# Performance work log

Measured on AMD Instinct MI355X. Metric: run time of the kernel, lower is better.

## Reference

```python
import jax, jax.numpy as jnp
import numpy as np

B, QL, KL = 2, 1024, 4096
H = 1024          # hidden_size
NH = 16           # num_heads
HD = H // NH      # head_dim = 64


def setup_inputs() -> dict:
    key = jax.random.key(0)
    k1, k2, k3, k4, k5 = jax.random.split(key, 5)
    s = 1.0 / np.sqrt(H)
    return {
        "query": jax.random.normal(k1, (B, QL, H), dtype=jnp.float32),
        "key_value": jax.random.normal(k2, (B, KL, H), dtype=jnp.float32),
        "w_q": jax.random.uniform(k3, (H, H), dtype=jnp.float32, minval=-s, maxval=s),
        "w_kv": jax.random.uniform(k4, (H, 2 * H), dtype=jnp.float32, minval=-s, maxval=s),
        "w_out": jax.random.uniform(k5, (H, H), dtype=jnp.float32, minval=-s, maxval=s),
    }


def reference(query, key_value, w_q, w_kv, w_out):
    # projections
    q = (query @ w_q).reshape(B, QL, NH, HD).transpose(0, 2, 1, 3)      # [B,NH,QL,HD]
    kv = (key_value @ w_kv).reshape(B, KL, 2, NH, HD)
    k = kv[:, :, 0].transpose(0, 2, 1, 3)                               # [B,NH,KL,HD]
    v = kv[:, :, 1].transpose(0, 2, 1, 3)                               # [B,NH,KL,HD]
    # scaled dot-product attention (explicit, matching source)
    scale = 1.0 / np.sqrt(HD).astype(np.float32)
    attn = jnp.einsum("bhqd,bhkd->bhqk", q, k) * scale                  # [B,NH,QL,KL]
    attn = jax.nn.softmax(attn, axis=-1)
    out = jnp.einsum("bhqk,bhkd->bhqd", attn, v)                        # [B,NH,QL,HD]
    out = out.transpose(0, 2, 1, 3).reshape(B, QL, H)
    return out @ w_out
```

## Files before the change

### kernel.cpp

```cpp
#include <hip/hip_runtime.h>

#define Bb   2
#define QL   1024
#define KL   4096
#define Hh   1024
#define NH   16
#define HD   64

#define KSPLIT 2
#define CHUNK  (KL / KSPLIT)
#define NTT    (CHUNK / 64)

typedef unsigned short u16;
typedef __attribute__((ext_vector_type(8))) short bf16x8;
typedef __attribute__((ext_vector_type(8))) unsigned short usv8;
typedef __attribute__((ext_vector_type(4))) float f32x4;

#define QSCALE 0.1803368801111204f
#define RTHR   11.0f

__device__ __forceinline__ u16 f2bf(float f) {
    union { float f; unsigned int u; } v; v.f = f;
    unsigned int r = (v.u + 0x7FFFu + ((v.u >> 16) & 1u)) >> 16;
    return (u16)r;
}

__device__ __forceinline__ unsigned int cvt_pk_bf16(float lo, float hi) {
    unsigned int r;
    asm("v_cvt_pk_bf16_f32 %0, %1, %2" : "=v"(r) : "v"(lo), "v"(hi));
    return r;
}

__device__ __forceinline__ float max3f(float a, float b, float c) {
    float r;
    asm("v_max3_f32 %0, %1, %2, %3" : "=v"(r) : "v"(a), "v"(b), "v"(c));
    return r;
}

__device__ __forceinline__ void gload16(const void* g, void* l) {
    __builtin_amdgcn_global_load_lds(
        (const __attribute__((address_space(1))) void*)g,
        (__attribute__((address_space(3))) void*)l, 16, 0, 0);
}

__device__ __forceinline__ uint4 pack8(const float4& f0, const float4& f1) {
    uint4 o;
    o.x = cvt_pk_bf16(f0.x, f0.y);
    o.y = cvt_pk_bf16(f0.z, f0.w);
    o.z = cvt_pk_bf16(f1.x, f1.y);
    o.w = cvt_pk_bf16(f1.z, f1.w);
    return o;
}

__global__ __launch_bounds__(256) void wtrans_all(const float* __restrict__ wq,
                                                  const float* __restrict__ wkv,
                                                  const float* __restrict__ wout,
                                                  u16* __restrict__ wqT,
                                                  u16* __restrict__ wkvT,
                                                  u16* __restrict__ woutT) {
    __shared__ float T[64][65];
    int bid = blockIdx.x;
    const float* in; u16* out; int C;
    if (bid < 256)      { in = wq;   out = wqT;   C = 1024; }
    else if (bid < 768) { in = wkv;  out = wkvT;  C = 2048; bid -= 256; }
    else                { in = wout; out = woutT; C = 1024; bid -= 768; }
    const int nc = C >> 6;
    const int c0 = (bid % nc) * 64;
    const int r0 = (bid / nc) * 64;
    const int t  = threadIdx.x;
    const int tx = t & 15, ty = t >> 4;
#pragma unroll
    for (int p = 0; p < 4; ++p) {
        const int r = ty + p * 16;
        float4 v = *reinterpret_cast<const float4*>(in + (size_t)(r0 + r) * C + c0 + tx * 4);
        T[r][tx * 4 + 0] = v.x; T[r][tx * 4 + 1] = v.y;
        T[r][tx * 4 + 2] = v.z; T[r][tx * 4 + 3] = v.w;
    }
    __syncthreads();
#pragma unroll
    for (int p = 0; p < 4; ++p) {
        const int c = ty + p * 16;
        const int n = c0 + c;
        ushort4 o;
        o.x = f2bf(T[tx * 4 + 0][c]); o.y = f2bf(T[tx * 4 + 1][c]);
        o.z = f2bf(T[tx * 4 + 2][c]); o.w = f2bf(T[tx * 4 + 3][c]);
        const int kb   = r0 + tx * 4;
        const int kout = (kb & ~63) | ((((kb >> 3) & 7) ^ (n & 7)) << 3) | (kb & 7);
        *reinterpret_cast<ushort4*>(out + (size_t)n * 1024 + kout) = o;
    }
}

__global__ __launch_bounds__(256) void qgemm(const float* __restrict__ A32,
                                             const u16* __restrict__ Bt,
                                             u16* __restrict__ C) {
    __shared__ u16 As[64 * 64];
    __shared__ u16 Bs[128 * 64];
    const int nwg = gridDim.x * gridDim.y;
    const int id  = blockIdx.y * gridDim.x + blockIdx.x;
    const int sw  = (id & 7) * (nwg >> 3) + (id >> 3);
    const int bx  = sw % gridDim.x, by = sw / gridDim.x;
    const int tid = threadIdx.x, lane = tid & 63, w = tid >> 6;
    const int wr = w >> 1, wc = w & 1;
    const int row0 = by * 64, col0 = bx * 128;
    const int MROW = wr * 32;
    const int x7   = lane & 7;

    f32x4 acc[2][4];
#pragma unroll
    for (int m = 0; m < 2; ++m)
#pragma unroll
        for (int n = 0; n < 4; ++n) acc[m][n] = (f32x4){0.f, 0.f, 0.f, 0.f};

    const int lrow = lane >> 3, lcol = (lane & 7) * 8;
    const int arow = tid >> 3, acol8 = (tid & 7) * 8;
    const int aphys = acol8 ^ ((arow & 7) << 3);

    for (int k0 = 0; k0 < 1024; k0 += 64) {
        __syncthreads();
#pragma unroll
        for (int p = 0; p < 2; ++p) {
            const int r = p * 32 + arow;
            const float* src = A32 + (size_t)(row0 + r) * 1024 + k0 + acol8;
            float4 f0 = *reinterpret_cast<const float4*>(src);
            float4 f1 = *reinterpret_cast<const float4*>(src + 4);
            *reinterpret_cast<uint4*>(&As[r * 64 + aphys]) = pack8(f0, f1);
        }
#pragma unroll
        for (int p = 0; p < 4; ++p) {
            const int base = w * 512 + p * 2048;
            const int row  = (base >> 6) + lrow;
            gload16(Bt + (size_t)(col0 + row) * 1024 + k0 + lcol, &Bs[base]);
        }
        __syncthreads();
#pragma unroll
        for (int kk = 0; kk < 2; ++kk) {
            bf16x8 af[2], bfr[4];
            const int G = ((kk * 4 + (lane >> 4)) ^ x7) * 8;
#pragma unroll
            for (int m = 0; m < 2; ++m)
                af[m] = *reinterpret_cast<const bf16x8*>(
                    &As[(MROW + m * 16 + (lane & 15)) * 64 + G]);
#pragma unroll
            for (int n = 0; n < 4; ++n)
                bfr[n] = *reinterpret_cast<const bf16x8*>(
                    &Bs[(wc * 64 + n * 16 + (lane & 15)) * 64 + G]);
#pragma unroll
            for (int m = 0; m < 2; ++m)
#pragma unroll
                for (int n = 0; n < 4; ++n)
                    acc[m][n] = __builtin_amdgcn_mfma_f32_16x16x32_bf16(
                        af[m], bfr[n], acc[m][n], 0, 0, 0);
        }
    }
#pragma unroll
    for (int m = 0; m < 2; ++m)
#pragma unroll
        for (int n = 0; n < 4; ++n) {
            const int gc = col0 + wc * 64 + n * 16 + (lane & 15);
#pragma unroll
            for (int r = 0; r < 4; ++r) {
                const int gr = row0 + MROW + m * 16 + (lane >> 4) * 4 + r;
                C[(size_t)gr * 1024 + gc] = f2bf(acc[m][n][r] * QSCALE);
            }
        }
}

__global__ __launch_bounds__(256) void kvgemm(const float* __restrict__ A32,
                                              const u16* __restrict__ Bt,
                                              u16* __restrict__ KT,
                                              u16* __restrict__ VT) {
    __shared__ u16 As[128 * 64];
    __shared__ u16 Bs[128 * 64];
    const int nwg = gridDim.x * gridDim.y;
    const int id  = blockIdx.y * gridDim.x + blockIdx.x;
    const int sw  = (id & 7) * (nwg >> 3) + (id >> 3);
    const int bx  = sw % gridDim.x, by = sw / gridDim.x;
    const int tid = threadIdx.x, lane = tid & 63, w = tid >> 6;
    const int wr = w >> 1, wc = w & 1;
    const int row0 = by * 128, col0 = bx * 128;
    const int MROW = wr * 64;
    const int x7   = lane & 7;

    f32x4 acc[4][4];
#pragma unroll
    for (int m = 0; m < 4; ++m)
#pragma unroll
        for (int n = 0; n < 4; ++n) acc[m][n] = (f32x4){0.f, 0.f, 0.f, 0.f};

    const int lrow = lane >> 3, lcol = (lane & 7) * 8;
    const int arow = tid >> 3, acol8 = (tid & 7) * 8;
    const int aphys = acol8 ^ ((arow & 7) << 3);

    auto stage = [&](int k0) {
        __syncthreads();
#pragma unroll
        for (int p = 0; p < 4; ++p) {
            const int r = p * 32 + arow;
            const float* src = A32 + (size_t)(row0 + r) * 1024 + k0 + acol8;
            float4 f0 = *reinterpret_cast<const float4*>(src);
            float4 f1 = *reinterpret_cast<const float4*>(src + 4);
            *reinterpret_cast<uint4*>(&As[r * 64 + aphys]) = pack8(f0, f1);
        }
#pragma unroll
        for (int p = 0; p < 4; ++p) {
            const int base = w * 512 + p * 2048;
            const int row  = (base >> 6) + lrow;
            gload16(Bt + (size_t)(col0 + row) * 1024 + k0 + lcol, &Bs[base]);
        }
        __syncthreads();
    };

    if (col0 < 1024) {
        for (int k0 = 0; k0 < 1024; k0 += 64) {
            stage(k0);
#pragma unroll
            for (int kk = 0; kk < 2; ++kk) {
                bf16x8 af[4], bfr[4];
                const int G = ((kk * 4 + (lane >> 4)) ^ x7) * 8;
#pragma unroll
                for (int m = 0; m < 4; ++m)
                    af[m] = *reinterpret_cast<const bf16x8*>(
                        &As[(MROW + m * 16 + (lane & 15)) * 64 + G]);
#pragma unroll
                for (int n = 0; n < 4; ++n)
                    bfr[n] = *reinterpret_cast<const bf16x8*>(
                        &Bs[(wc * 64 + n * 16 + (lane & 15)) * 64 + G]);
#pragma unroll
                for (int m = 0; m < 4; ++m)
#pragma unroll
                    for (int n = 0; n < 4; ++n)
                        acc[m][n] = __builtin_amdgcn_mfma_f32_16x16x32_bf16(
                            bfr[n], af[m], acc[m][n], 0, 0, 0);
            }
        }
#pragma unroll
        for (int m = 0; m < 4; ++m) {
            const int gr  = row0 + MROW + m * 16 + (lane & 15);
            const int b   = gr >> 12;
            const int k   = gr & 4095;
            const int kt_i = k >> 6, k_in = k & 63;
#pragma unroll
            for (int n = 0; n < 4; ++n) {
                const int gc0 = col0 + wc * 64 + n * 16 + (lane >> 4) * 4;
                const int h   = gc0 >> 6, d0 = gc0 & 63;
                u16* blob = KT + (((size_t)((b << 4) + h) * 64 + kt_i) << 9) * 8;
                const int og = k_in * 8 + ((d0 >> 3) ^ (k_in & 7));
                ushort4 pk;
                pk.x = f2bf(acc[m][n][0]); pk.y = f2bf(acc[m][n][1]);
                pk.z = f2bf(acc[m][n][2]); pk.w = f2bf(acc[m][n][3]);
                *reinterpret_cast<ushort4*>(&blob[og * 8 + (d0 & 7)]) = pk;
            }
        }
    } else {
        for (int k0 = 0; k0 < 1024; k0 += 64) {
            stage(k0);
#pragma unroll
            for (int kk = 0; kk < 2; ++kk) {
                bf16x8 af[4], bfr[4];
                const int G = ((kk * 4 + (lane >> 4)) ^ x7) * 8;
#pragma unroll
                for (int m = 0; m < 4; ++m)
                    af[m] = *reinterpret_cast<const bf16x8*>(
                        &As[(MROW + m * 16 + (lane & 15)) * 64 + G]);
#pragma unroll
                for (int n = 0; n < 4; ++n)
                    bfr[n] = *reinterpret_cast<const bf16x8*>(
                        &Bs[(wc * 64 + n * 16 + (lane & 15)) * 64 + G]);
#pragma unroll
                for (int m = 0; m < 4; ++m)
#pragma unroll
                    for (int n = 0; n < 4; ++n)
                        acc[m][n] = __builtin_amdgcn_mfma_f32_16x16x32_bf16(
                            af[m], bfr[n], acc[m][n], 0, 0, 0);
            }
        }
#pragma unroll
        for (int m = 0; m < 4; ++m) {
            const int gr0 = row0 + MROW + m * 16 + (lane >> 4) * 4;
            const int b   = gr0 >> 12;
            const int k   = gr0 & 4095;
            const int kt_i = k >> 6, k_in = k & 63;
#pragma unroll
            for (int n = 0; n < 4; ++n) {
                const int gc = col0 + wc * 64 + n * 16 + (lane & 15);
                const int h  = (gc & 1023) >> 6, d = gc & 63;
                u16* blob = VT + (((size_t)((b << 4) + h) * 64 + kt_i) << 9) * 8;
                const int og = d * 8 + ((k_in >> 3) ^ (d & 7));
                ushort4 pk;
                pk.x = f2bf(acc[m][n][0]); pk.y = f2bf(acc[m][n][1]);
                pk.z = f2bf(acc[m][n][2]); pk.w = f2bf(acc[m][n][3]);
                *reinterpret_cast<ushort4*>(&blob[og * 8 + (k_in & 7)]) = pk;
            }
        }
    }
}

__global__ __launch_bounds__(256, 4) void attn_mfma(const u16* __restrict__ Qb,
                                                    const u16* __restrict__ KT,
                                                    const u16* __restrict__ VT2,
                                                    float* __restrict__ Op,
                                                    float* __restrict__ m_ws,
                                                    float* __restrict__ l_ws) {
    __shared__ u16 Ks[2][64 * 64];
    __shared__ u16 Vs[2][64 * 64];
    __shared__ u16 Ps[4][16][64];

    const int bid0 = blockIdx.x;
    const int bid  = (bid0 & 7) * 128 + (bid0 >> 3);
    const int qb   = bid & 15;
    const int h    = (bid >> 4) & 15;
    const int b    = (bid >> 8) & 1;
    const int c    = bid >> 9;
    const int tid  = threadIdx.x;
    const int lane = tid & 63;
    const int w    = tid >> 6;
    const int q_l  = lane & 15;
    const int g    = lane >> 4;
    const int qs7  = q_l & 7;
    const int q0   = qb * 64;
    const int bh   = b * NH + h;

    bf16x8 qa0, qa1;
    {
        const u16* qsrc = Qb + (size_t)(b * QL + q0 + w * 16 + q_l) * Hh
                          + h * HD + g * 8;
        qa0 = *reinterpret_cast<const bf16x8*>(qsrc);
        qa1 = *reinterpret_cast<const bf16x8*>(qsrc + 32);
    }
    asm volatile("s_waitcnt vmcnt(0)" ::: "memory");

    bf16x8 ones;
#pragma unroll
    for (int e = 0; e < 8; ++e) ones[e] = (short)0x3F80;

    float m_i = -1e30f;
    f32x4 acc_l = (f32x4){0.f, 0.f, 0.f, 0.f};
    f32x4 acc_o[4];
#pragma unroll
    for (int n = 0; n < 4; ++n) acc_o[n] = (f32x4){0.f, 0.f, 0.f, 0.f};

    const size_t tb0 = ((size_t)bh * 64 + c * NTT) * 512 * 8;
    const u16* kq = KT  + tb0;
    const u16* vq = VT2 + tb0;

    auto issue = [&](const u16* kptr, const u16* vptr, int bufi) {
#pragma unroll
        for (int p = 0; p < 2; ++p)
            gload16(kptr + (size_t)(p * 256 + w * 64 + lane) * 8,
                    &Ks[bufi][(p * 256 + w * 64) * 8]);
#pragma unroll
        for (int p = 0; p < 2; ++p)
            gload16(vptr + (size_t)(p * 256 + w * 64 + lane) * 8,
                    &Vs[bufi][(p * 256 + w * 64) * 8]);
    };

    issue(kq, vq, 0);

    for (int t = 0; t < NTT; ++t) {
        const int cur = t & 1;
        __builtin_amdgcn_s_barrier();
        if (t + 1 < NTT) {
            kq += 4096; vq += 4096;
            issue(kq, vq, cur ^ 1);
            asm volatile("s_waitcnt vmcnt(4)" ::: "memory");
        } else {
            asm volatile("s_waitcnt vmcnt(0)" ::: "memory");
        }
        __builtin_amdgcn_sched_barrier(0);
        __builtin_amdgcn_s_barrier();

        f32x4 s[4];
        __builtin_amdgcn_s_setprio(1);
#pragma unroll
        for (int n = 0; n < 4; ++n) {
            const int r_ = n * 16 + q_l;
            bf16x8 a0 = *reinterpret_cast<const bf16x8*>(
                &Ks[cur][r_ * 64 + (g ^ qs7) * 8]);
            bf16x8 a1 = *reinterpret_cast<const bf16x8*>(
                &Ks[cur][r_ * 64 + ((g + 4) ^ qs7) * 8]);
            f32x4 z = (f32x4){0.f, 0.f, 0.f, 0.f};
            z = __builtin_amdgcn_mfma_f32_16x16x32_bf16(a0, qa0, z, 0, 0, 0);
            z = __builtin_amdgcn_mfma_f32_16x16x32_bf16(a1, qa1, z, 0, 0, 0);
            s[n] = z;
        }
        __builtin_amdgcn_s_setprio(0);

        float c1 = max3f(s[0][0], s[0][1], s[0][2]);
        c1 = max3f(c1, s[0][3], s[1][0]);
        c1 = max3f(c1, s[1][1], s[1][2]);
        c1 = fmaxf(c1, s[1][3]);
        float c2 = max3f(s[2][0], s[2][1], s[2][2]);
        c2 = max3f(c2, s[2][3], s[3][0]);
        c2 = max3f(c2, s[3][1], s[3][2]);
        c2 = fmaxf(c2, s[3][3]);
        float mloc = fmaxf(c1, c2);
        mloc = fmaxf(mloc, __shfl_xor(mloc, 16));
        mloc = fmaxf(mloc, __shfl_xor(mloc, 32));

        if (__any(mloc > m_i + RTHR)) {
            const float mnew = fmaxf(m_i, mloc);
            const float al   = exp2f(m_i - mnew);
            m_i = mnew;
            acc_l[0] *= al; acc_l[1] *= al; acc_l[2] *= al; acc_l[3] *= al;
#pragma unroll
            for (int n = 0; n < 4; ++n) {
                f32x4 tt = acc_o[n];
                tt[0] *= al; tt[1] *= al; tt[2] *= al; tt[3] *= al;
                acc_o[n] = tt;
            }
        }
#pragma unroll
        for (int n = 0; n < 4; ++n)
#pragma unroll
            for (int r = 0; r < 4; ++r) s[n][r] = exp2f(s[n][r] - m_i);

#pragma unroll
        for (int n = 0; n < 4; ++n) {
            uint2 pk2;
            pk2.x = cvt_pk_bf16(s[n][0], s[n][1]);
            pk2.y = cvt_pk_bf16(s[n][2], s[n][3]);
            const int phys = (2 * n + (g >> 1)) ^ qs7;
            *reinterpret_cast<uint2*>(&Ps[w][q_l][phys * 8 + (g & 1) * 4]) = pk2;
        }
        asm volatile("s_waitcnt lgkmcnt(0)" ::: "memory");
        __builtin_amdgcn_sched_barrier(0);

        __builtin_amdgcn_s_setprio(1);
#pragma unroll
        for (int kf = 0; kf < 2; ++kf) {
            const int phk = ((kf * 4 + g) ^ qs7) * 8;
            bf16x8 pfr = *reinterpret_cast<const bf16x8*>(&Ps[w][q_l][phk]);
            acc_l = __builtin_amdgcn_mfma_f32_16x16x32_bf16(ones, pfr, acc_l, 0, 0, 0);
#pragma unroll
            for (int n = 0; n < 4; ++n) {
                const int d_ = n * 16 + q_l;
                bf16x8 vf = *reinterpret_cast<const bf16x8*>(
                    &Vs[cur][d_ * 64 + phk]);
                acc_o[n] = __builtin_amdgcn_mfma_f32_16x16x32_bf16(
                    vf, pfr, acc_o[n], 0, 0, 0);
            }
        }
        __builtin_amdgcn_s_setprio(0);
    }

    float* opc = Op + (size_t)c * ((size_t)Bb * QL * Hh)
                 + (size_t)(b * QL + q0 + w * 16 + q_l) * Hh + h * HD;
#pragma unroll
    for (int n = 0; n < 4; ++n) {
        float4 v = make_float4(acc_o[n][0], acc_o[n][1], acc_o[n][2], acc_o[n][3]);
        *reinterpret_cast<float4*>(opc + n * 16 + g * 4) = v;
    }
    if (g == 0) {
        const int idx = ((c * Bb + b) * NH + h) * QL + q0 + w * 16 + q_l;
        m_ws[idx] = m_i;
        l_ws[idx] = acc_l[0];
    }
}

__global__ __launch_bounds__(256) void ogemm(const float* __restrict__ Op,
                                             const float* __restrict__ m_ws,
                                             const float* __restrict__ l_ws,
                                             const u16* __restrict__ Bt,
                                             float* __restrict__ C) {
    __shared__ u16 As[64 * 64];
    __shared__ u16 Bs[128 * 64];
    const int nwg = gridDim.x * gridDim.y;
    const int id  = blockIdx.y * gridDim.x + blockIdx.x;
    const int sw  = (id & 7) * (nwg >> 3) + (id >> 3);
    const int bx  = sw % gridDim.x, by = sw / gridDim.x;
    const int tid = threadIdx.x, lane = tid & 63, w = tid >> 6;
    const int wr = w >> 1, wc = w & 1;
    const int row0 = by * 64, col0 = bx * 128;
    const int MROW = wr * 32;
    const int x7   = lane & 7;

    f32x4 acc[2][4];
#pragma unroll
    for (int m = 0; m < 2; ++m)
#pragma unroll
        for (int n = 0; n < 4; ++n) acc[m][n] = (f32x4){0.f, 0.f, 0.f, 0.f};

    const int lrow = lane >> 3, lcol = (lane & 7) * 8;
    const int arow = tid >> 3, acol8 = (tid & 7) * 8;
    const int aphys = acol8 ^ ((arow & 7) << 3);

    for (int k0 = 0; k0 < 1024; k0 += 64) {
        __syncthreads();
        const int h_ = k0 >> 6;
#pragma unroll
        for (int p = 0; p < 2; ++p) {
            const int r    = p * 32 + arow;
            const int grow = row0 + r;
            const int b_   = grow >> 10, q_ = grow & 1023;
            const int idx  = (((b_ << 4) + h_) << 10) + q_;
            const float m0 = m_ws[idx], m1 = m_ws[idx + 32768];
            const float l0 = l_ws[idx], l1 = l_ws[idx + 32768];
            const float ms = fmaxf(m0, m1);
            float a0 = exp2f(m0 - ms), a1 = exp2f(m1 - ms);
            const float inv = 1.f / (l0 * a0 + l1 * a1);
            a0 *= inv; a1 *= inv;
            const float* o0 = Op + (size_t)grow * 1024 + k0 + acol8;
            const float* o1 = o0 + (size_t)Bb * QL * Hh;
            float4 x0 = *reinterpret_cast<const float4*>(o0);
            float4 x1 = *reinterpret_cast<const float4*>(o0 + 4);
            float4 y0 = *reinterpret_cast<const float4*>(o1);
            float4 y1 = *reinterpret_cast<const float4*>(o1 + 4);
            float4 f0 = make_float4(x0.x * a0 + y0.x * a1, x0.y * a0 + y0.y * a1,
                                    x0.z * a0 + y0.z * a1, x0.w * a0 + y0.w * a1);
            float4 f1 = make_float4(x1.x * a0 + y1.x * a1, x1.y * a0 + y1.y * a1,
                                    x1.z * a0 + y1.z * a1, x1.w * a0 + y1.w * a1);
            *reinterpret_cast<uint4*>(&As[r * 64 + aphys]) = pack8(f0, f1);
        }
#pragma unroll
        for (int p = 0; p < 4; ++p) {
            const int base = w * 512 + p * 2048;
            const int row  = (base >> 6) + lrow;
            gload16(Bt + (size_t)(col0 + row) * 1024 + k0 + lcol, &Bs[base]);
        }
        __syncthreads();
#pragma unroll
        for (int kk = 0; kk < 2; ++kk) {
            bf16x8 af[2], bfr[4];
            const int G = ((kk * 4 + (lane >> 4)) ^ x7) * 8;
#pragma unroll
            for (int m = 0; m < 2; ++m)
                af[m] = *reinterpret_cast<const bf16x8*>(
                    &As[(MROW + m * 16 + (lane & 15)) * 64 + G]);
#pragma unroll
            for (int n = 0; n < 4; ++n)
                bfr[n] = *reinterpret_cast<const bf16x8*>(
                    &Bs[(wc * 64 + n * 16 + (lane & 15)) * 64 + G]);
#pragma unroll
            for (int m = 0; m < 2; ++m)
#pragma unroll
                for (int n = 0; n < 4; ++n)
                    acc[m][n] = __builtin_amdgcn_mfma_f32_16x16x32_bf16(
                        af[m], bfr[n], acc[m][n], 0, 0, 0);
        }
    }
#pragma unroll
    for (int m = 0; m < 2; ++m)
#pragma unroll
        for (int n = 0; n < 4; ++n) {
            const int gc = col0 + wc * 64 + n * 16 + (lane & 15);
#pragma unroll
            for (int r = 0; r < 4; ++r) {
                const int gr = row0 + MROW + m * 16 + (lane >> 4) * 4 + r;
                C[(size_t)gr * 1024 + gc] = acc[m][n][r];
            }
        }
}

extern "C" void kernel_launch(void* const* d_in, const int* in_sizes, int n_in,
                              void* d_out, int out_size, void* d_ws, size_t ws_size,
                              hipStream_t stream) {
    const float* query     = (const float*)d_in[0];
    const float* key_value = (const float*)d_in[1];
    const float* w_q       = (const float*)d_in[2];
    const float* w_kv      = (const float*)d_in[3];
    const float* w_out     = (const float*)d_in[4];
    float* out = (float*)d_out;

    char* ws = (char*)d_ws;
    const size_t MB = 1024 * 1024;
    u16*   KT    = (u16*)(ws);
    u16*   VT    = (u16*)(ws + 16 * MB);
    float* Opart = (float*)(ws + 32 * MB);
    u16*   Qb    = (u16*)(ws + 48 * MB);
    u16*   wkvT  = (u16*)(ws + 52 * MB);
    u16*   wqT   = (u16*)(ws + 56 * MB);
    u16*   woutT = (u16*)(ws + 58 * MB);
    float* m_wsp = (float*)(ws + 60 * MB);
    float* l_wsp = (float*)(ws + 60 * MB + 256 * 1024);

    dim3 blk(256);

    wtrans_all<<<1024, blk, 0, stream>>>(w_q, w_kv, w_out, wqT, wkvT, woutT);

    qgemm<<<dim3(8, 32), blk, 0, stream>>>(query, wqT, Qb);

    kvgemm<<<dim3(16, 64), blk, 0, stream>>>(key_value, wkvT, KT, VT);

    attn_mfma<<<dim3(KSPLIT * 512), blk, 0, stream>>>(
        Qb, KT, VT, Opart, m_wsp, l_wsp);

    ogemm<<<dim3(8, 32), blk, 0, stream>>>(Opart, m_wsp, l_wsp, woutT, out);
}
```

Baseline: 183.7 us.

## Process two query sub-tiles per wave in attention to reuse K/V fragments

Each attention block now covers 128 query rows instead of 64, with each wave handling two 16-row query sub-tiles that share the same K and V LDS fragment loads. This halves the grid and the global K/V traffic per query, and lowers LDS reads per MFMA. LDS addresses are precomputed as pointers and the loop is unrolled by two to fix the buffer index. The cost is roughly double the accumulator registers (launch bounds go from 4 to 2 waves per SIMD) and fewer blocks, which lowers occupancy and leaves less latency hiding.

```diff
diff --git a/kernel.cpp b/kernel.cpp
--- a/kernel.cpp
+++ b/kernel.cpp
@@ -295,37 +295,38 @@
     }
 }
 
-__global__ __launch_bounds__(256, 4) void attn_mfma(const u16* __restrict__ Qb,
+__global__ __launch_bounds__(256, 2) void attn_mfma(const u16* __restrict__ Qb,
                                                     const u16* __restrict__ KT,
                                                     const u16* __restrict__ VT2,
                                                     float* __restrict__ Op,
                                                     float* __restrict__ m_ws,
                                                     float* __restrict__ l_ws) {
-    __shared__ u16 Ks[2][64 * 64];
-    __shared__ u16 Vs[2][64 * 64];
-    __shared__ u16 Ps[4][16][64];
+    __shared__ u16 Ks[2][4096];
+    __shared__ u16 Vs[2][4096];
+    __shared__ u16 Ps[4][2][1024];
 
     const int bid0 = blockIdx.x;
-    const int bid  = (bid0 & 7) * 128 + (bid0 >> 3);
-    const int qb   = bid & 15;
-    const int h    = (bid >> 4) & 15;
-    const int b    = (bid >> 8) & 1;
-    const int c    = bid >> 9;
+    const int bid  = (bid0 & 7) * 64 + (bid0 >> 3);
+    const int qb   = bid & 7;
+    const int h    = (bid >> 3) & 15;
+    const int b    = (bid >> 7) & 1;
+    const int c    = bid >> 8;
     const int tid  = threadIdx.x;
     const int lane = tid & 63;
     const int w    = tid >> 6;
     const int q_l  = lane & 15;
     const int g    = lane >> 4;
     const int qs7  = q_l & 7;
-    const int q0   = qb * 64;
+    const int q0   = qb * 128;
     const int bh   = b * NH + h;
 
-    bf16x8 qa0, qa1;
-    {
-        const u16* qsrc = Qb + (size_t)(b * QL + q0 + w * 16 + q_l) * Hh
+    bf16x8 qa[2][2];
+#pragma unroll
+    for (int qh = 0; qh < 2; ++qh) {
+        const u16* qsrc = Qb + (size_t)(b * QL + q0 + w * 32 + qh * 16 + q_l) * Hh
                           + h * HD + g * 8;
-        qa0 = *reinterpret_cast<const bf16x8*>(qsrc);
-        qa1 = *reinterpret_cast<const bf16x8*>(qsrc + 32);
+        qa[qh][0] = *reinterpret_cast<const bf16x8*>(qsrc);
+        qa[qh][1] = *reinterpret_cast<const bf16x8*>(qsrc + 32);
     }
     asm volatile("s_waitcnt vmcnt(0)" ::: "memory");
 
@@ -333,35 +334,47 @@
 #pragma unroll
     for (int e = 0; e < 8; ++e) ones[e] = (short)0x3F80;
 
-    float m_i = -1e30f;
-    f32x4 acc_l = (f32x4){0.f, 0.f, 0.f, 0.f};
-    f32x4 acc_o[4];
-#pragma unroll
-    for (int n = 0; n < 4; ++n) acc_o[n] = (f32x4){0.f, 0.f, 0.f, 0.f};
-
-    const size_t tb0 = ((size_t)bh * 64 + c * NTT) * 512 * 8;
-    const u16* kq = KT  + tb0;
-    const u16* vq = VT2 + tb0;
-
-    auto issue = [&](const u16* kptr, const u16* vptr, int bufi) {
-#pragma unroll
-        for (int p = 0; p < 2; ++p)
-            gload16(kptr + (size_t)(p * 256 + w * 64 + lane) * 8,
-                    &Ks[bufi][(p * 256 + w * 64) * 8]);
-#pragma unroll
-        for (int p = 0; p < 2; ++p)
-            gload16(vptr + (size_t)(p * 256 + w * 64 + lane) * 8,
-                    &Vs[bufi][(p * 256 + w * 64) * 8]);
-    };
-
-    issue(kq, vq, 0);
-
-    for (int t = 0; t < NTT; ++t) {
-        const int cur = t & 1;
+    float m_i[2] = {-1e30f, -1e30f};
+    f32x4 acc_l[2] = {(f32x4){0.f, 0.f, 0.f, 0.f}, (f32x4){0.f, 0.f, 0.f, 0.f}};
+    f32x4 acc_o[2][4];
+#pragma unroll
+    for (int qh = 0; qh < 2; ++qh)
+#pragma unroll
+        for (int n = 0; n < 4; ++n) acc_o[qh][n] = (f32x4){0.f, 0.f, 0.f, 0.f};
+
+    const int koffA = (g ^ qs7) * 8;
+    const int koffB = ((g + 4) ^ qs7) * 8;
+    const int rowq  = q_l * 64;
+    const u16* KsA[2] = { &Ks[0][rowq + koffA], &Ks[1][rowq + koffA] };
+    const u16* KsB[2] = { &Ks[0][rowq + koffB], &Ks[1][rowq + koffB] };
+    const u16* VsA[2] = { &Vs[0][rowq + koffA], &Vs[1][rowq + koffA] };
+    const u16* VsB[2] = { &Vs[0][rowq + koffB], &Vs[1][rowq + koffB] };
+    const u16* PsRA = &Ps[w][0][rowq + koffA];
+    const u16* PsRB = &Ps[w][0][rowq + koffB];
+    u16* PsW[4];
+#pragma unroll
+    for (int n = 0; n < 4; ++n)
+        PsW[n] = &Ps[w][0][rowq + (((2 * n + (g >> 1)) ^ qs7) << 3) + (g & 1) * 4];
+
+    const size_t tb0 = ((size_t)bh * 64 + c * NTT) * 4096;
+    const u16* kpt = KT  + tb0 + (size_t)(w * 64 + lane) * 8 + 1024;
+    const u16* vpt = VT2 + tb0 + (size_t)(w * 64 + lane) * 8 + 1024;
+    u16* kdst[2] = { &Ks[0][w * 512], &Ks[1][w * 512] };
+    u16* vdst[2] = { &Vs[0][w * 512], &Vs[1][w * 512] };
+
+    gload16(kpt - 1024, kdst[0]);
+    gload16(kpt + 1024, kdst[0] + 2048);
+    gload16(vpt - 1024, vdst[0]);
+    gload16(vpt + 1024, vdst[0] + 2048);
+
+    auto tile = [&](int CUR, int t) {
         __builtin_amdgcn_s_barrier();
         if (t + 1 < NTT) {
-            kq += 4096; vq += 4096;
-            issue(kq, vq, cur ^ 1);
+            kpt += 4096; vpt += 4096;
+            gload16(kpt - 1024, kdst[CUR ^ 1]);
+            gload16(kpt + 1024, kdst[CUR ^ 1] + 2048);
+            gload16(vpt - 1024, vdst[CUR ^ 1]);
+            gload16(vpt + 1024, vdst[CUR ^ 1] + 2048);
             asm volatile("s_waitcnt vmcnt(4)" ::: "memory");
         } else {
             asm volatile("s_waitcnt vmcnt(0)" ::: "memory");
@@ -369,58 +382,67 @@
         __builtin_amdgcn_sched_barrier(0);
         __builtin_amdgcn_s_barrier();
 
-        f32x4 s[4];
+        f32x4 s[2][4];
         __builtin_amdgcn_s_setprio(1);
 #pragma unroll
         for (int n = 0; n < 4; ++n) {
-            const int r_ = n * 16 + q_l;
-            bf16x8 a0 = *reinterpret_cast<const bf16x8*>(
-                &Ks[cur][r_ * 64 + (g ^ qs7) * 8]);
-            bf16x8 a1 = *reinterpret_cast<const bf16x8*>(
-                &Ks[cur][r_ * 64 + ((g + 4) ^ qs7) * 8]);
-            f32x4 z = (f32x4){0.f, 0.f, 0.f, 0.f};
-            z = __builtin_amdgcn_mfma_f32_16x16x32_bf16(a0, qa0, z, 0, 0, 0);
-            z = __builtin_amdgcn_mfma_f32_16x16x32_bf16(a1, qa1, z, 0, 0, 0);
-            s[n] = z;
+            bf16x8 a0 = *reinterpret_cast<const bf16x8*>(KsA[CUR] + n * 1024);
+            bf16x8 a1 = *reinterpret_cast<const bf16x8*>(KsB[CUR] + n * 1024);
+#pragma unroll
+            for (int qh = 0; qh < 2; ++qh) {
+                f32x4 z = (f32x4){0.f, 0.f, 0.f, 0.f};
+                z = __builtin_amdgcn_mfma_f32_16x16x32_bf16(a0, qa[qh][0], z, 0, 0, 0);
+                z = __builtin_amdgcn_mfma_f32_16x16x32_bf16(a1, qa[qh][1], z, 0, 0, 0);
+                s[qh][n] = z;
+            }
         }
         __builtin_amdgcn_s_setprio(0);
 
-        float c1 = max3f(s[0][0], s[0][1], s[0][2]);
-        c1 = max3f(c1, s[0][3], s[1][0]);
-        c1 = max3f(c1, s[1][1], s[1][2]);
-        c1 = fmaxf(c1, s[1][3]);
-        float c2 = max3f(s[2][0], s[2][1], s[2][2]);
-        c2 = max3f(c2, s[2][3], s[3][0]);
-        c2 = max3f(c2, s[3][1], s[3][2]);
-        c2 = fmaxf(c2, s[3][3]);
-        float mloc = fmaxf(c1, c2);
-        mloc = fmaxf(mloc, __shfl_xor(mloc, 16));
-        mloc = fmaxf(mloc, __shfl_xor(mloc, 32));
-
-        if (__any(mloc > m_i + RTHR)) {
-            const float mnew = fmaxf(m_i, mloc);
-            const float al   = exp2f(m_i - mnew);
-            m_i = mnew;
-            acc_l[0] *= al; acc_l[1] *= al; acc_l[2] *= al; acc_l[3] *= al;
+        float mloc[2];
+#pragma unroll
+        for (int qh = 0; qh < 2; ++qh) {
+            float c1 = max3f(s[qh][0][0], s[qh][0][1], s[qh][0][2]);
+            c1 = max3f(c1, s[qh][0][3], s[qh][1][0]);
+            c1 = max3f(c1, s[qh][1][1], s[qh][1][2]);
+            c1 = fmaxf(c1, s[qh][1][3]);
+            float c2 = max3f(s[qh][2][0], s[qh][2][1], s[qh][2][2]);
+            c2 = max3f(c2, s[qh][2][3], s[qh][3][0]);
+            c2 = max3f(c2, s[qh][3][1], s[qh][3][2]);
+            c2 = fmaxf(c2, s[qh][3][3]);
+            float m = fmaxf(c1, c2);
+            m = fmaxf(m, __shfl_xor(m, 16));
+            m = fmaxf(m, __shfl_xor(m, 32));
+            mloc[qh] = m;
+        }
+        if (__any((mloc[0] > m_i[0] + RTHR) || (mloc[1] > m_i[1] + RTHR))) {
+#pragma unroll
+            for (int qh = 0; qh < 2; ++qh) {
+                const float mnew = fmaxf(m_i[qh], mloc[qh]);
+                const float al   = exp2f(m_i[qh] - mnew);
+                m_i[qh] = mnew;
+                acc_l[qh][0] *= al; acc_l[qh][1] *= al;
+                acc_l[qh][2] *= al; acc_l[qh][3] *= al;
+#pragma unroll
+                for (int n = 0; n < 4; ++n) {
+                    f32x4 tt = acc_o[qh][n];
+                    tt[0] *= al; tt[1] *= al; tt[2] *= al; tt[3] *= al;
+                    acc_o[qh][n] = tt;
+                }
+            }
+        }
+#pragma unroll
+        for (int qh = 0; qh < 2; ++qh) {
+#pragma unroll
+            for (int n = 0; n < 4; ++n)
+#pragma unroll
+                for (int r = 0; r < 4; ++r) s[qh][n][r] = exp2f(s[qh][n][r] - m_i[qh]);
 #pragma unroll
             for (int n = 0; n < 4; ++n) {
-                f32x4 tt = acc_o[n];
-                tt[0] *= al; tt[1] *= al; tt[2] *= al; tt[3] *= al;
-                acc_o[n] = tt;
-            }
-        }
-#pragma unroll
-        for (int n = 0; n < 4; ++n)
-#pragma unroll
-            for (int r = 0; r < 4; ++r) s[n][r] = exp2f(s[n][r] - m_i);
-
-#pragma unroll
-        for (int n = 0; n < 4; ++n) {
-            uint2 pk2;
-            pk2.x = cvt_pk_bf16(s[n][0], s[n][1]);
-            pk2.y = cvt_pk_bf16(s[n][2], s[n][3]);
-            const int phys = (2 * n + (g >> 1)) ^ qs7;
-            *reinterpret_cast<uint2*>(&Ps[w][q_l][phys * 8 + (g & 1) * 4]) = pk2;
+                uint2 pk2;
+                pk2.x = cvt_pk_bf16(s[qh][n][0], s[qh][n][1]);
+                pk2.y = cvt_pk_bf16(s[qh][n][2], s[qh][n][3]);
+                *reinterpret_cast<uint2*>(PsW[n] + qh * 1024) = pk2;
+            }
         }
         asm volatile("s_waitcnt lgkmcnt(0)" ::: "memory");
         __builtin_amdgcn_sched_barrier(0);
@@ -428,32 +450,42 @@
         __builtin_amdgcn_s_setprio(1);
 #pragma unroll
         for (int kf = 0; kf < 2; ++kf) {
-            const int phk = ((kf * 4 + g) ^ qs7) * 8;
-            bf16x8 pfr = *reinterpret_cast<const bf16x8*>(&Ps[w][q_l][phk]);
-            acc_l = __builtin_amdgcn_mfma_f32_16x16x32_bf16(ones, pfr, acc_l, 0, 0, 0);
+            const u16* pr = (kf == 0) ? PsRA : PsRB;
+            bf16x8 pf0 = *reinterpret_cast<const bf16x8*>(pr);
+            bf16x8 pf1 = *reinterpret_cast<const bf16x8*>(pr + 1024);
+            acc_l[0] = __builtin_amdgcn_mfma_f32_16x16x32_bf16(ones, pf0, acc_l[0], 0, 0, 0);
+            acc_l[1] = __builtin_amdgcn_mfma_f32_16x16x32_bf16(ones, pf1, acc_l[1], 0, 0, 0);
 #pragma unroll
             for (int n = 0; n < 4; ++n) {
-                const int d_ = n * 16 + q_l;
-                bf16x8 vf = *reinterpret_cast<const bf16x8*>(
-                    &Vs[cur][d_ * 64 + phk]);
-                acc_o[n] = __builtin_amdgcn_mfma_f32_16x16x32_bf16(
-                    vf, pfr, acc_o[n], 0, 0, 0);
+                const u16* vb = (kf == 0) ? VsA[CUR] : VsB[CUR];
+                bf16x8 vf = *reinterpret_cast<const bf16x8*>(vb + n * 1024);
+                acc_o[0][n] = __builtin_amdgcn_mfma_f32_16x16x32_bf16(vf, pf0, acc_o[0][n], 0, 0, 0);
+                acc_o[1][n] = __builtin_amdgcn_mfma_f32_16x16x32_bf16(vf, pf1, acc_o[1][n], 0, 0, 0);
             }
         }
         __builtin_amdgcn_s_setprio(0);
-    }
-
-    float* opc = Op + (size_t)c * ((size_t)Bb * QL * Hh)
-                 + (size_t)(b * QL + q0 + w * 16 + q_l) * Hh + h * HD;
-#pragma unroll
-    for (int n = 0; n < 4; ++n) {
-        float4 v = make_float4(acc_o[n][0], acc_o[n][1], acc_o[n][2], acc_o[n][3]);
-        *reinterpret_cast<float4*>(opc + n * 16 + g * 4) = v;
-    }
-    if (g == 0) {
-        const int idx = ((c * Bb + b) * NH + h) * QL + q0 + w * 16 + q_l;
-        m_ws[idx] = m_i;
-        l_ws[idx] = acc_l[0];
+    };
+
+    for (int t = 0; t < NTT; t += 2) {
+        tile(0, t);
+        tile(1, t + 1);
+    }
+
+#pragma unroll
+    for (int qh = 0; qh < 2; ++qh) {
+        float* opc = Op + (size_t)c * ((size_t)Bb * QL * Hh)
+                     + (size_t)(b * QL + q0 + w * 32 + qh * 16 + q_l) * Hh + h * HD;
+#pragma unroll
+        for (int n = 0; n < 4; ++n) {
+            float4 v = make_float4(acc_o[qh][n][0], acc_o[qh][n][1],
+                                   acc_o[qh][n][2], acc_o[qh][n][3]);
+            *reinterpret_cast<float4*>(opc + n * 16 + g * 4) = v;
+        }
+        if (g == 0) {
+            const int idx = ((c * Bb + b) * NH + h) * QL + q0 + w * 32 + qh * 16 + q_l;
+            m_ws[idx] = m_i[qh];
+            l_ws[idx] = acc_l[qh][0];
+        }
     }
 }
 
@@ -581,7 +613,7 @@
 
     kvgemm<<<dim3(16, 64), blk, 0, stream>>>(key_value, wkvT, KT, VT);
 
-    attn_mfma<<<dim3(KSPLIT * 512), blk, 0, stream>>>(
+    attn_mfma<<<dim3(KSPLIT * 256), blk, 0, stream>>>(
         Qb, KT, VT, Opart, m_wsp, l_wsp);
 
     ogemm<<<dim3(8, 32), blk, 0, stream>>>(Opart, m_wsp, l_wsp, woutT, out);
```

Measured after the change: 186.0 us. No clear change (+1.3%).

## Double KV tile size in attention and register-prefetch A in kvgemm

Applied to the files above, without the earlier changes.

The attention kernel now processes 128-key tiles per iteration instead of 64, doubling the LDS buffers and halving the number of barriers and waits per chunk. It also precomputes LDS pointers and unrolls the double-buffer loop by two so buffer indices are compile-time constants. Occupancy is lowered to 2 blocks per CU to fit the larger shared memory and register use. kvgemm now prefetches the next fp32 A tile into registers while the current tile computes, using raw s_barrier and explicit waitcnts instead of __syncthreads, and declares 4 blocks per CU.

```diff
diff --git a/kernel.cpp b/kernel.cpp
--- a/kernel.cpp
+++ b/kernel.cpp
@@ -9,7 +9,7 @@
 
 #define KSPLIT 2
 #define CHUNK  (KL / KSPLIT)
-#define NTT    (CHUNK / 64)
+#define NTM    (CHUNK / 128)
 
 typedef unsigned short u16;
 typedef __attribute__((ext_vector_type(8))) short bf16x8;
@@ -165,10 +165,10 @@
         }
 }
 
-__global__ __launch_bounds__(256) void kvgemm(const float* __restrict__ A32,
-                                              const u16* __restrict__ Bt,
-                                              u16* __restrict__ KT,
-                                              u16* __restrict__ VT) {
+__global__ __launch_bounds__(256, 4) void kvgemm(const float* __restrict__ A32,
+                                                 const u16* __restrict__ Bt,
+                                                 u16* __restrict__ KT,
+                                                 u16* __restrict__ VT) {
     __shared__ u16 As[128 * 64];
     __shared__ u16 Bs[128 * 64];
     const int nwg = gridDim.x * gridDim.y;
@@ -190,49 +190,76 @@
     const int lrow = lane >> 3, lcol = (lane & 7) * 8;
     const int arow = tid >> 3, acol8 = (tid & 7) * 8;
     const int aphys = acol8 ^ ((arow & 7) << 3);
-
-    auto stage = [&](int k0) {
-        __syncthreads();
-#pragma unroll
-        for (int p = 0; p < 4; ++p) {
-            const int r = p * 32 + arow;
-            const float* src = A32 + (size_t)(row0 + r) * 1024 + k0 + acol8;
-            float4 f0 = *reinterpret_cast<const float4*>(src);
-            float4 f1 = *reinterpret_cast<const float4*>(src + 4);
-            *reinterpret_cast<uint4*>(&As[r * 64 + aphys]) = pack8(f0, f1);
-        }
+    const float* abase = A32 + (size_t)(row0 + arow) * 1024 + acol8;
+
+    float4 ar[8];
+#pragma unroll
+    for (int p = 0; p < 4; ++p) {
+        const float* src = abase + (size_t)p * 32 * 1024;
+        ar[2 * p]     = *reinterpret_cast<const float4*>(src);
+        ar[2 * p + 1] = *reinterpret_cast<const float4*>(src + 4);
+    }
+
+    auto step = [&](int k0, bool kmode) {
+        __builtin_amdgcn_s_barrier();
+#pragma unroll
+        for (int p = 0; p < 4; ++p)
+            *reinterpret_cast<uint4*>(&As[(p * 32 + arow) * 64 + aphys]) =
+                pack8(ar[2 * p], ar[2 * p + 1]);
 #pragma unroll
         for (int p = 0; p < 4; ++p) {
             const int base = w * 512 + p * 2048;
             const int row  = (base >> 6) + lrow;
             gload16(Bt + (size_t)(col0 + row) * 1024 + k0 + lcol, &Bs[base]);
         }
-        __syncthreads();
-    };
-
-    if (col0 < 1024) {
-        for (int k0 = 0; k0 < 1024; k0 += 64) {
-            stage(k0);
-#pragma unroll
-            for (int kk = 0; kk < 2; ++kk) {
-                bf16x8 af[4], bfr[4];
-                const int G = ((kk * 4 + (lane >> 4)) ^ x7) * 8;
-#pragma unroll
-                for (int m = 0; m < 4; ++m)
-                    af[m] = *reinterpret_cast<const bf16x8*>(
-                        &As[(MROW + m * 16 + (lane & 15)) * 64 + G]);
-#pragma unroll
-                for (int n = 0; n < 4; ++n)
-                    bfr[n] = *reinterpret_cast<const bf16x8*>(
-                        &Bs[(wc * 64 + n * 16 + (lane & 15)) * 64 + G]);
+        __builtin_amdgcn_sched_barrier(0);
+        if (k0 + 64 < 1024) {
+#pragma unroll
+            for (int p = 0; p < 4; ++p) {
+                const float* src = abase + (size_t)p * 32 * 1024 + (k0 + 64);
+                ar[2 * p]     = *reinterpret_cast<const float4*>(src);
+                ar[2 * p + 1] = *reinterpret_cast<const float4*>(src + 4);
+            }
+            __builtin_amdgcn_sched_barrier(0);
+            asm volatile("s_waitcnt vmcnt(8)" ::: "memory");
+        } else {
+            asm volatile("s_waitcnt vmcnt(0)" ::: "memory");
+        }
+        asm volatile("s_waitcnt lgkmcnt(0)" ::: "memory");
+        __builtin_amdgcn_sched_barrier(0);
+        __builtin_amdgcn_s_barrier();
+#pragma unroll
+        for (int kk = 0; kk < 2; ++kk) {
+            bf16x8 af[4], bfr[4];
+            const int G = ((kk * 4 + (lane >> 4)) ^ x7) * 8;
+#pragma unroll
+            for (int m = 0; m < 4; ++m)
+                af[m] = *reinterpret_cast<const bf16x8*>(
+                    &As[(MROW + m * 16 + (lane & 15)) * 64 + G]);
+#pragma unroll
+            for (int n = 0; n < 4; ++n)
+                bfr[n] = *reinterpret_cast<const bf16x8*>(
+                    &Bs[(wc * 64 + n * 16 + (lane & 15)) * 64 + G]);
+            if (kmode) {
 #pragma unroll
                 for (int m = 0; m < 4; ++m)
 #pragma unroll
                     for (int n = 0; n < 4; ++n)
                         acc[m][n] = __builtin_amdgcn_mfma_f32_16x16x32_bf16(
                             bfr[n], af[m], acc[m][n], 0, 0, 0);
-            }
-        }
+            } else {
+#pragma unroll
+                for (int m = 0; m < 4; ++m)
+#pragma unroll
+                    for (int n = 0; n < 4; ++n)
+                        acc[m][n] = __builtin_amdgcn_mfma_f32_16x16x32_bf16(
+                            af[m], bfr[n], acc[m][n], 0, 0, 0);
+            }
+        }
+    };
+
+    if (col0 < 1024) {
+        for (int k0 = 0; k0 < 1024; k0 += 64) step(k0, true);
 #pragma unroll
         for (int m = 0; m < 4; ++m) {
             const int gr  = row0 + MROW + m * 16 + (lane & 15);
@@ -252,28 +279,7 @@
             }
         }
     } else {
-        for (int k0 = 0; k0 < 1024; k0 += 64) {
-            stage(k0);
-#pragma unroll
-            for (int kk = 0; kk < 2; ++kk) {
-                bf16x8 af[4], bfr[4];
-                const int G = ((kk * 4 + (lane >> 4)) ^ x7) * 8;
-#pragma unroll
-                for (int m = 0; m < 4; ++m)
-                    af[m] = *reinterpret_cast<const bf16x8*>(
-                        &As[(MROW + m * 16 + (lane & 15)) * 64 + G]);
-#pragma unroll
-                for (int n = 0; n < 4; ++n)
-                    bfr[n] = *reinterpret_cast<const bf16x8*>(
-                        &Bs[(wc * 64 + n * 16 + (lane & 15)) * 64 + G]);
-#pragma unroll
-                for (int m = 0; m < 4; ++m)
-#pragma unroll
-                    for (int n = 0; n < 4; ++n)
-                        acc[m][n] = __builtin_amdgcn_mfma_f32_16x16x32_bf16(
-                            af[m], bfr[n], acc[m][n], 0, 0, 0);
-            }
-        }
+        for (int k0 = 0; k0 < 1024; k0 += 64) step(k0, false);
 #pragma unroll
         for (int m = 0; m < 4; ++m) {
             const int gr0 = row0 + MROW + m * 16 + (lane >> 4) * 4;
@@ -295,15 +301,15 @@
     }
 }
 
-__global__ __launch_bounds__(256, 4) void attn_mfma(const u16* __restrict__ Qb,
+__global__ __launch_bounds__(256, 2) void attn_mfma(const u16* __restrict__ Qb,
                                                     const u16* __restrict__ KT,
                                                     const u16* __restrict__ VT2,
                                                     float* __restrict__ Op,
                                                     float* __restrict__ m_ws,
                                                     float* __restrict__ l_ws) {
-    __shared__ u16 Ks[2][64 * 64];
-    __shared__ u16 Vs[2][64 * 64];
-    __shared__ u16 Ps[4][16][64];
+    __shared__ u16 Ks[2 * 8192];
+    __shared__ u16 Vs[2 * 8192];
+    __shared__ u16 Ps[4 * 2048];
 
     const int bid0 = blockIdx.x;
     const int bid  = (bid0 & 7) * 128 + (bid0 >> 3);
@@ -339,45 +345,58 @@
 #pragma unroll
     for (int n = 0; n < 4; ++n) acc_o[n] = (f32x4){0.f, 0.f, 0.f, 0.f};
 
-    const size_t tb0 = ((size_t)bh * 64 + c * NTT) * 512 * 8;
-    const u16* kq = KT  + tb0;
-    const u16* vq = VT2 + tb0;
-
-    auto issue = [&](const u16* kptr, const u16* vptr, int bufi) {
-#pragma unroll
-        for (int p = 0; p < 2; ++p)
-            gload16(kptr + (size_t)(p * 256 + w * 64 + lane) * 8,
-                    &Ks[bufi][(p * 256 + w * 64) * 8]);
-#pragma unroll
-        for (int p = 0; p < 2; ++p)
-            gload16(vptr + (size_t)(p * 256 + w * 64 + lane) * 8,
-                    &Vs[bufi][(p * 256 + w * 64) * 8]);
+    const int koffA = (g ^ qs7) * 8;
+    const int koffB = ((g + 4) ^ qs7) * 8;
+    const int rowq  = q_l * 64;
+    const u16* kA[2] = { &Ks[rowq + koffA], &Ks[8192 + rowq + koffA] };
+    const u16* kB[2] = { &Ks[rowq + koffB], &Ks[8192 + rowq + koffB] };
+    const u16* vA[2] = { &Vs[rowq + koffA], &Vs[8192 + rowq + koffA] };
+    const u16* vB[2] = { &Vs[rowq + koffB], &Vs[8192 + rowq + koffB] };
+    const u16* pA = &Ps[w * 2048 + rowq + koffA];
+    const u16* pB = &Ps[w * 2048 + rowq + koffB];
+    u16* PsW[4];
+#pragma unroll
+    for (int n = 0; n < 4; ++n)
+        PsW[n] = &Ps[w * 2048 + rowq + (((2 * n + (g >> 1)) ^ qs7) << 3) + (g & 1) * 4];
+
+    const size_t tb0 = ((size_t)bh * 64 + c * (CHUNK / 64)) * 4096;
+    const u16* kq = KT  + tb0 + (size_t)(w * 64 + lane) * 8;
+    const u16* vq = VT2 + tb0 + (size_t)(w * 64 + lane) * 8;
+    u16* kd[2] = { &Ks[w * 512], &Ks[8192 + w * 512] };
+    u16* vd[2] = { &Vs[w * 512], &Vs[8192 + w * 512] };
+
+    auto issue8 = [&](const u16* kp, const u16* vp, int bufi) {
+        gload16(kp,        kd[bufi]);
+        gload16(kp + 2048, kd[bufi] + 2048);
+        gload16(kp + 4096, kd[bufi] + 4096);
+        gload16(kp + 6144, kd[bufi] + 6144);
+        gload16(vp,        vd[bufi]);
+        gload16(vp + 2048, vd[bufi] + 2048);
+        gload16(vp + 4096, vd[bufi] + 4096);
+        gload16(vp + 6144, vd[bufi] + 6144);
     };
 
-    issue(kq, vq, 0);
-
-    for (int t = 0; t < NTT; ++t) {
-        const int cur = t & 1;
+    issue8(kq, vq, 0);
+
+    auto tile = [&](int CUR, int t) {
+        const int B0 = CUR * 8192;
         __builtin_amdgcn_s_barrier();
-        if (t + 1 < NTT) {
-            kq += 4096; vq += 4096;
-            issue(kq, vq, cur ^ 1);
-            asm volatile("s_waitcnt vmcnt(4)" ::: "memory");
+        if (t + 1 < NTM) {
+            kq += 8192; vq += 8192;
+            issue8(kq, vq, CUR ^ 1);
+            asm volatile("s_waitcnt vmcnt(8)" ::: "memory");
         } else {
             asm volatile("s_waitcnt vmcnt(0)" ::: "memory");
         }
         __builtin_amdgcn_sched_barrier(0);
         __builtin_amdgcn_s_barrier();
 
-        f32x4 s[4];
+        f32x4 s[8];
         __builtin_amdgcn_s_setprio(1);
 #pragma unroll
-        for (int n = 0; n < 4; ++n) {
-            const int r_ = n * 16 + q_l;
-            bf16x8 a0 = *reinterpret_cast<const bf16x8*>(
-                &Ks[cur][r_ * 64 + (g ^ qs7) * 8]);
-            bf16x8 a1 = *reinterpret_cast<const bf16x8*>(
-                &Ks[cur][r_ * 64 + ((g + 4) ^ qs7) * 8]);
+        for (int n = 0; n < 8; ++n) {
+            bf16x8 a0 = *reinterpret_cast<const bf16x8*>(kA[CUR] + n * 1024);
+            bf16x8 a1 = *reinterpret_cast<const bf16x8*>(kB[CUR] + n * 1024);
             f32x4 z = (f32x4){0.f, 0.f, 0.f, 0.f};
             z = __builtin_amdgcn_mfma_f32_16x16x32_bf16(a0, qa0, z, 0, 0, 0);
             z = __builtin_amdgcn_mfma_f32_16x16x32_bf16(a1, qa1, z, 0, 0, 0);
@@ -385,20 +404,16 @@
         }
         __builtin_amdgcn_s_setprio(0);
 
-        float c1 = max3f(s[0][0], s[0][1], s[0][2]);
-        c1 = max3f(c1, s[0][3], s[1][0]);
-        c1 = max3f(c1, s[1][1], s[1][2]);
-        c1 = fmaxf(c1, s[1][3]);
-        float c2 = max3f(s[2][0], s[2][1], s[2][2]);
-        c2 = max3f(c2, s[2][3], s[3][0]);
-        c2 = max3f(c2, s[3][1], s[3][2]);
-        c2 = fmaxf(c2, s[3][3]);
-        float mloc = fmaxf(c1, c2);
-        mloc = fmaxf(mloc, __shfl_xor(mloc, 16));
-        mloc = fmaxf(mloc, __shfl_xor(mloc, 32));
-
-        if (__any(mloc > m_i + RTHR)) {
-            const float mnew = fmaxf(m_i, mloc);
+        float mx = max3f(s[0][0], s[0][1], s[0][2]);
+#pragma unroll
+        for (int i = 3; i + 1 < 32; i += 2)
+            mx = max3f(mx, s[i >> 2][i & 3], s[(i + 1) >> 2][(i + 1) & 3]);
+        mx = fmaxf(mx, s[7][3]);
+        mx = fmaxf(mx, __shfl_xor(mx, 16));
+        mx = fmaxf(mx, __shfl_xor(mx, 32));
+
+        if (__any(mx > m_i + RTHR)) {
+            const float mnew = fmaxf(m_i, mx);
             const float al   = exp2f(m_i - mnew);
             m_i = mnew;
             acc_l[0] *= al; acc_l[1] *= al; acc_l[2] *= al; acc_l[3] *= al;
@@ -410,37 +425,41 @@
             }
         }
 #pragma unroll
-        for (int n = 0; n < 4; ++n)
+        for (int n = 0; n < 8; ++n)
 #pragma unroll
             for (int r = 0; r < 4; ++r) s[n][r] = exp2f(s[n][r] - m_i);
 
 #pragma unroll
-        for (int n = 0; n < 4; ++n) {
+        for (int n = 0; n < 8; ++n) {
             uint2 pk2;
             pk2.x = cvt_pk_bf16(s[n][0], s[n][1]);
             pk2.y = cvt_pk_bf16(s[n][2], s[n][3]);
-            const int phys = (2 * n + (g >> 1)) ^ qs7;
-            *reinterpret_cast<uint2*>(&Ps[w][q_l][phys * 8 + (g & 1) * 4]) = pk2;
+            *reinterpret_cast<uint2*>(PsW[n & 3] + (n >> 2) * 1024) = pk2;
         }
         asm volatile("s_waitcnt lgkmcnt(0)" ::: "memory");
         __builtin_amdgcn_sched_barrier(0);
 
         __builtin_amdgcn_s_setprio(1);
 #pragma unroll
-        for (int kf = 0; kf < 2; ++kf) {
-            const int phk = ((kf * 4 + g) ^ qs7) * 8;
-            bf16x8 pfr = *reinterpret_cast<const bf16x8*>(&Ps[w][q_l][phk]);
+        for (int kf = 0; kf < 4; ++kf) {
+            const int sub = kf >> 1;
+            const u16* pr = ((kf & 1) ? pB : pA) + sub * 1024;
+            bf16x8 pfr = *reinterpret_cast<const bf16x8*>(pr);
             acc_l = __builtin_amdgcn_mfma_f32_16x16x32_bf16(ones, pfr, acc_l, 0, 0, 0);
+            const u16* vb = ((kf & 1) ? vB[CUR] : vA[CUR]) + sub * 4096;
 #pragma unroll
             for (int n = 0; n < 4; ++n) {
-                const int d_ = n * 16 + q_l;
-                bf16x8 vf = *reinterpret_cast<const bf16x8*>(
-                    &Vs[cur][d_ * 64 + phk]);
+                bf16x8 vf = *reinterpret_cast<const bf16x8*>(vb + n * 1024);
                 acc_o[n] = __builtin_amdgcn_mfma_f32_16x16x32_bf16(
                     vf, pfr, acc_o[n], 0, 0, 0);
             }
         }
         __builtin_amdgcn_s_setprio(0);
+    };
+
+    for (int t = 0; t < NTM; t += 2) {
+        tile(0, t);
+        tile(1, t + 1);
     }
 
     float* opc = Op + (size_t)c * ((size_t)Bb * QL * Hh)
```

Measured after the change: 238.3 us. 1.3x slower.
